# Kernel tuning notes

Measured on AMD Instinct MI355X. Metric: run time of the kernel, lower is better.

## Reference

```python
import jax, jax.numpy as jnp
import numpy as np
from jax import lax

B, S, D = 16, 1024, 1024
PE = 20          # positioning_embedding (LSTM hidden)
NB = 3           # num_building_blocks
EPS = 1e-12      # F.normalize eps


def setup_inputs() -> dict:
    key = jax.random.key(0)
    ks = jax.random.split(key, 10)
    s = lambda *sh: 0.05
    inp = {
        "x": jax.random.normal(ks[0], (B, S, D), dtype=jnp.float32),
        # LSTM params (PyTorch layout: gates ordered i,f,g,o)
        "W_ih": jax.random.normal(ks[1], (4 * PE, D), dtype=jnp.float32) * 0.02,
        "W_hh": jax.random.normal(ks[2], (4 * PE, PE), dtype=jnp.float32) * 0.02,
        "b_ih": jax.random.normal(ks[3], (4 * PE,), dtype=jnp.float32) * 0.02,
        "b_hh": jax.random.normal(ks[4], (4 * PE,), dtype=jnp.float32) * 0.02,
        # mu_generator: Linear(PE -> NB)
        "W_mu": jax.random.normal(ks[5], (NB, PE), dtype=jnp.float32) * 0.1,
        "b_mu": jax.random.normal(ks[6], (NB,), dtype=jnp.float32) * 0.1,
        # sigma_generator: Linear(PE -> 1)
        "W_sig": jax.random.normal(ks[7], (1, PE), dtype=jnp.float32) * 0.1,
        "b_sig": jax.random.normal(ks[8], (1,), dtype=jnp.float32) * 0.1,
    }
    return inp


def _lstm(x, W_ih, W_hh, b_ih, b_hh):
    # x: [B, S, D] -> h: [B, S, PE]; single-layer batch_first LSTM, h0=c0=0
    b, _, _ = x.shape
    H = W_hh.shape[1]
    xg = jnp.einsum("bsd,gd->bsg", x, W_ih) + b_ih + b_hh  # [B,S,4H]

    def step(carry, xg_t):
        h, c = carry
        g = xg_t + h @ W_hh.T
        i, f, gg, o = jnp.split(g, 4, axis=-1)
        c = jax.nn.sigmoid(f) * c + jax.nn.sigmoid(i) * jnp.tanh(gg)
        h = jax.nn.sigmoid(o) * jnp.tanh(c)
        return (h, c), h

    init = (jnp.zeros((b, H), x.dtype), jnp.zeros((b, H), x.dtype))
    _, hs = lax.scan(step, init, xg.transpose(1, 0, 2))  # hs: [S,B,H]
    return hs.transpose(1, 0, 2)


def _forward(x, W_ih, W_hh, b_ih, b_hh, W_mu, b_mu, W_sig, b_sig):
    b, s, d = x.shape
    pw = _lstm(x, W_ih, W_hh, b_ih, b_hh)                       # [B,S,PE]
    mu_w = jax.nn.relu(jnp.einsum("bsp,np->bsn", pw, W_mu) + b_mu)   # [B,S,3]
    sigma = jax.nn.sigmoid(jnp.einsum("bsp,op->bso", pw, W_sig) + b_sig)[..., 0]  # [B,S]

    # sequential mu recurrence: mu_j = w0*prev_mu + w1*(1/S) + w2*(j+1)/S
    j_idx = jnp.arange(s, dtype=x.dtype)

    def mu_step(prev_mu, inputs):
        w_t, j = inputs  # w_t: [B,3]
        mu = w_t[:, 0] * prev_mu + w_t[:, 1] / s + w_t[:, 2] * (j + 1.0) / s
        return mu, mu

    _, mus = lax.scan(mu_step, jnp.zeros((b,), x.dtype),
                      (mu_w.transpose(1, 0, 2), j_idx))          # mus: [S,B]
    mu = mus.T                                                    # [B,S]

    # triangular relative positions: rel[j,i] = i/(j+1) for i<=j
    i_idx = jnp.arange(s, dtype=x.dtype)
    rel = i_idx[None, :] / (j_idx[:, None] + 1.0)                 # [S,S]
    mask = i_idx[None, :] <= j_idx[:, None]                       # lower-triangular

    w = jnp.exp(-((rel[None] - mu[:, :, None]) ** 2)
                / (2.0 * sigma[:, :, None] ** 2))                 # [B,S,S]
    w = jnp.where(mask[None], w, 0.0)
    # F.normalize over the position axis (L2)
    norm = jnp.sqrt(jnp.sum(w * w, axis=-1, keepdims=True))
    w = w / jnp.maximum(norm, EPS)

    context = jnp.einsum("bji,bid->bjd", w, x)                    # [B,S,D]
    return context


def reference(x, W_ih, W_hh, b_ih, b_hh, W_mu, b_mu, W_sig, b_sig):
    return _forward(x, W_ih, W_hh, b_ih, b_hh, W_mu, b_mu, W_sig, b_sig)
```

## Files before the change

### kernel.cpp

```cpp
#include <hip/hip_runtime.h>

#define DEVFN __device__ __forceinline__

static constexpr int cB  = 16;
static constexpr int cS  = 1024;
static constexpr int cD  = 1024;
static constexpr int cPE = 20;
static constexpr int cG  = 80;

typedef float  floatx2  __attribute__((ext_vector_type(2)));
typedef float  floatx4  __attribute__((ext_vector_type(4)));
typedef float  floatx16 __attribute__((ext_vector_type(16)));
typedef short  short8   __attribute__((ext_vector_type(8)));
typedef unsigned uintx2 __attribute__((ext_vector_type(2)));

DEVFN unsigned pack_bf(float a, float b) {
  union { float f; unsigned u; } ua, ub; ua.f = a; ub.f = b;
  return (ua.u >> 16) | (ub.u & 0xffff0000u);
}

static constexpr int K1_XS = 68;

__global__ __launch_bounds__(256) void k1_xg(
    const float* __restrict__ x, const float* __restrict__ W_ih,
    const float* __restrict__ b_ih, const float* __restrict__ b_hh,
    float* __restrict__ xgT, unsigned short* __restrict__ xbf_t, int use_bf)
{
  __shared__ float xs[64 * K1_XS];
  __shared__ float wsm[80 * K1_XS];

  const int t  = threadIdx.x;
  const int rg = t >> 4, cg = t & 15;
  const int r0 = rg * 4, c0 = cg * 5;
  const int row0 = blockIdx.x * 64;
  const int b  = row0 >> 10;
  const int s0 = row0 & 1023;

  floatx2 acc[4][5];
#pragma unroll
  for (int q = 0; q < 4; ++q)
#pragma unroll
    for (int cc = 0; cc < 5; ++cc) { acc[q][cc].x = 0.f; acc[q][cc].y = 0.f; }

  for (int kc = 0; kc < 16; ++kc) {
    const int k0 = kc * 64;
    {
      const int sr = t >> 2, sc = t & 3;
      const float4* src = (const float4*)(x + (size_t)(row0 + sr) * cD + k0 + sc * 16);
      float4 v0 = src[0], v1 = src[1], v2 = src[2], v3 = src[3];
      float4* dst = (float4*)&xs[sr * K1_XS + sc * 16];
      dst[0] = v0; dst[1] = v1; dst[2] = v2; dst[3] = v3;
    }
#pragma unroll
    for (int q = 0; q < 5; ++q) {
      const int id = t + q * 256;
      const int g = id >> 4, c4 = id & 15;
      float4 wv = *(const float4*)(W_ih + (size_t)g * cD + k0 + c4 * 4);
      *(float4*)&wsm[g * K1_XS + c4 * 4] = wv;
    }
    __syncthreads();

    if (use_bf) {
      const int dl = t >> 2, sc4 = t & 3;
      float v[16];
#pragma unroll
      for (int e = 0; e < 16; ++e) v[e] = xs[(sc4 * 16 + e) * K1_XS + dl];
      unsigned u[8];
#pragma unroll
      for (int p = 0; p < 8; ++p) u[p] = pack_bf(v[2 * p], v[2 * p + 1]);
      unsigned short* dstp = xbf_t + ((size_t)(b * cD + k0 + dl)) * cS + s0 + sc4 * 16;
      *(uint4*)dstp       = make_uint4(u[0], u[1], u[2], u[3]);
      *(uint4*)(dstp + 8) = make_uint4(u[4], u[5], u[6], u[7]);
    }

#pragma unroll 4
    for (int k2 = 0; k2 < 32; ++k2) {
      floatx2 xv[4], wv[5];
#pragma unroll
      for (int q = 0; q < 4; ++q)
        xv[q] = *(const floatx2*)&xs[(r0 + q) * K1_XS + 2 * k2];
#pragma unroll
      for (int cc = 0; cc < 5; ++cc)
        wv[cc] = *(const floatx2*)&wsm[(c0 + cc) * K1_XS + 2 * k2];
#pragma unroll
      for (int q = 0; q < 4; ++q)
#pragma unroll
        for (int cc = 0; cc < 5; ++cc)
          acc[q][cc] += xv[q] * wv[cc];
    }
    __syncthreads();
  }

#pragma unroll
  for (int cc = 0; cc < 5; ++cc) {
    const int g = c0 + cc;
    const float sc = (g >= 40 && g < 60) ? 2.88539008f : 1.44269504f;
    const float bs = b_ih[g] + b_hh[g];
    float4 v;
    v.x = (acc[0][cc].x + acc[0][cc].y + bs) * sc;
    v.y = (acc[1][cc].x + acc[1][cc].y + bs) * sc;
    v.z = (acc[2][cc].x + acc[2][cc].y + bs) * sc;
    v.w = (acc[3][cc].x + acc[3][cc].y + bs) * sc;
    *(float4*)&xgT[((size_t)(b * cG + g)) * cS + s0 + r0] = v;
  }
}

__global__ __launch_bounds__(64) void k2_lstm(
    const float* __restrict__ xgT, const float* __restrict__ W_hh,
    float* __restrict__ hbuf)
{
  const int b    = blockIdx.x;
  const int lane = threadIdx.x;
  const int half = lane >> 5;
  const int l31  = lane & 31;
  const int j    = (l31 < cPE) ? l31 : (cPE - 1);
  const float LOG2E = 1.44269504f, TWOLOG2E = 2.88539008f;

  const int rowA = half ? (20 + j) : j;
  const int rowB = half ? (60 + j) : (40 + j);
  const float sB   = half ? LOG2E : TWOLOG2E;
  const float subB = half ? 0.f : 1.f;

  floatx2 wA[10], wB[10];
#pragma unroll
  for (int p = 0; p < 10; ++p) {
    wA[p].x = W_hh[rowA * cPE + 2 * p]     * LOG2E;
    wA[p].y = W_hh[rowA * cPE + 2 * p + 1] * LOG2E;
    wB[p].x = W_hh[rowB * cPE + 2 * p]     * sB;
    wB[p].y = W_hh[rowB * cPE + 2 * p + 1] * sB;
  }

  const float* baseA = xgT + ((size_t)(b * cG + rowA)) * cS;
  const float* baseB = xgT + ((size_t)(b * cG + rowB)) * cS;

  float4 bufA[4], bufB[4];
#pragma unroll
  for (int s = 0; s < 4; ++s) {
    bufA[s] = *(const float4*)(baseA + s * 4);
    bufB[s] = *(const float4*)(baseB + s * 4);
  }

  unsigned long long hp[10];
#pragma unroll
  for (int p = 0; p < 10; ++p) hp[p] = 0ull;

  float c = 0.f;
  float* hb = hbuf + (size_t)b * cS * cPE + j;

  for (int q0 = 0; q0 < 256; q0 += 4) {
#pragma unroll
    for (int s = 0; s < 4; ++s) {
      const int q = q0 + s;
      const float4 gA4 = bufA[s];
      const float4 gB4 = bufB[s];
      bufA[s] = *(const float4*)(baseA + (q + 4) * 4);
      bufB[s] = *(const float4*)(baseB + (q + 4) * 4);
#pragma unroll
      for (int e = 0; e < 4; ++e) {
        const float geA = (e == 0) ? gA4.x : (e == 1) ? gA4.y : (e == 2) ? gA4.z : gA4.w;
        const float geB = (e == 0) ? gB4.x : (e == 1) ? gB4.y : (e == 2) ? gB4.z : gB4.w;

        floatx2 aA0, aA1, aB0, aB1;
        aA0.x = geA; aA0.y = 0.f; aA1.x = 0.f; aA1.y = 0.f;
        aB0.x = geB; aB0.y = 0.f; aB1.x = 0.f; aB1.y = 0.f;
#pragma unroll
        for (int p = 0; p < 5; ++p) {
          asm("v_pk_fma_f32 %0, %1, %2, %0" : "+v"(aA0) : "v"(wA[p]),     "s"(hp[p]));
          asm("v_pk_fma_f32 %0, %1, %2, %0" : "+v"(aA1) : "v"(wA[5 + p]), "s"(hp[5 + p]));
          asm("v_pk_fma_f32 %0, %1, %2, %0" : "+v"(aB0) : "v"(wB[p]),     "s"(hp[p]));
          asm("v_pk_fma_f32 %0, %1, %2, %0" : "+v"(aB1) : "v"(wB[5 + p]), "s"(hp[5 + p]));
        }
        const float gAv = (aA0.x + aA0.y) + (aA1.x + aA1.y);
        const float gBv = (aB0.x + aB0.y) + (aB1.x + aB1.y);

        const float eA   = __builtin_amdgcn_exp2f(fminf(gAv, 30.f));
        const float actA = eA * __builtin_amdgcn_rcpf(eA + 1.f);
        const float eB   = __builtin_amdgcn_exp2f(fminf(gBv, 30.f));
        const float actB = (eB - subB) * __builtin_amdgcn_rcpf(eB + 1.f);

        union { float f; unsigned u; } ca, cb;
        ca.f = actA; cb.f = actB;
        uintx2 rA = __builtin_amdgcn_permlane32_swap(ca.u, ca.u, false, false);
        uintx2 rB = __builtin_amdgcn_permlane32_swap(cb.u, cb.u, false, false);
        union { unsigned u; float f; } vf, vi, vg, vo;
        vi.u = rA.x; vf.u = rA.y; vg.u = rB.x; vo.u = rB.y;

        c = vf.f * c + vi.f * vg.f;
        const float ec = __builtin_amdgcn_exp2f(fminf(TWOLOG2E * c, 30.f));
        const float th = (ec - 1.f) * __builtin_amdgcn_rcpf(ec + 1.f);
        const float hj = vo.f * th;

        if (lane < cPE) hb[(size_t)(q * 4 + e) * cPE] = hj;

        union { float f; unsigned u; } ch; ch.f = hj;
        const int hbits = (int)ch.u;
        const unsigned l0  = (unsigned)__builtin_amdgcn_readlane(hbits, 0);
        const unsigned l1  = (unsigned)__builtin_amdgcn_readlane(hbits, 1);
        const unsigned l2  = (unsigned)__builtin_amdgcn_readlane(hbits, 2);
        const unsigned l3  = (unsigned)__builtin_amdgcn_readlane(hbits, 3);
        const unsigned l4  = (unsigned)__builtin_amdgcn_readlane(hbits, 4);
        const unsigned l5  = (unsigned)__builtin_amdgcn_readlane(hbits, 5);
        const unsigned l6  = (unsigned)__builtin_amdgcn_readlane(hbits, 6);
        const unsigned l7  = (unsigned)__builtin_amdgcn_readlane(hbits, 7);
        const unsigned l8  = (unsigned)__builtin_amdgcn_readlane(hbits, 8);
        const unsigned l9  = (unsigned)__builtin_amdgcn_readlane(hbits, 9);
        const unsigned l10 = (unsigned)__builtin_amdgcn_readlane(hbits, 10);
        const unsigned l11 = (unsigned)__builtin_amdgcn_readlane(hbits, 11);
        const unsigned l12 = (unsigned)__builtin_amdgcn_readlane(hbits, 12);
        const unsigned l13 = (unsigned)__builtin_amdgcn_readlane(hbits, 13);
        const unsigned l14 = (unsigned)__builtin_amdgcn_readlane(hbits, 14);
        const unsigned l15 = (unsigned)__builtin_amdgcn_readlane(hbits, 15);
        const unsigned l16 = (unsigned)__builtin_amdgcn_readlane(hbits, 16);
        const unsigned l17 = (unsigned)__builtin_amdgcn_readlane(hbits, 17);
        const unsigned l18 = (unsigned)__builtin_amdgcn_readlane(hbits, 18);
        const unsigned l19 = (unsigned)__builtin_amdgcn_readlane(hbits, 19);
        hp[0] = (unsigned long long)l0  | ((unsigned long long)l1  << 32);
        hp[1] = (unsigned long long)l2  | ((unsigned long long)l3  << 32);
        hp[2] = (unsigned long long)l4  | ((unsigned long long)l5  << 32);
        hp[3] = (unsigned long long)l6  | ((unsigned long long)l7  << 32);
        hp[4] = (unsigned long long)l8  | ((unsigned long long)l9  << 32);
        hp[5] = (unsigned long long)l10 | ((unsigned long long)l11 << 32);
        hp[6] = (unsigned long long)l12 | ((unsigned long long)l13 << 32);
        hp[7] = (unsigned long long)l14 | ((unsigned long long)l15 << 32);
        hp[8] = (unsigned long long)l16 | ((unsigned long long)l17 << 32);
        hp[9] = (unsigned long long)l18 | ((unsigned long long)l19 << 32);
      }
    }
  }
}

__global__ __launch_bounds__(256) void k3a_muw(
    const float* __restrict__ hbuf,
    const float* __restrict__ W_mu, const float* __restrict__ b_mu,
    const float* __restrict__ W_sig, const float* __restrict__ b_sig,
    float* __restrict__ muwT, float* __restrict__ sigma)
{
  __shared__ float sw[84];
  const int t = threadIdx.x;
  if (t < 60) sw[t] = W_mu[t];
  else if (t < 80) sw[t] = W_sig[t - 60];
  else if (t < 83) sw[t] = b_mu[t - 80];
  else if (t == 83) sw[t] = b_sig[0];
  __syncthreads();

  const int r = blockIdx.x * 256 + t;
  const float4* hp = (const float4*)(hbuf + (size_t)r * cPE);
  float h[20];
#pragma unroll
  for (int q2 = 0; q2 < 5; ++q2) {
    float4 v = hp[q2];
    h[4 * q2] = v.x; h[4 * q2 + 1] = v.y; h[4 * q2 + 2] = v.z; h[4 * q2 + 3] = v.w;
  }
  float m0 = sw[80], m1 = sw[81], m2 = sw[82], sg = sw[83];
#pragma unroll
  for (int p = 0; p < 20; ++p) {
    m0 += sw[p]      * h[p];
    m1 += sw[20 + p] * h[p];
    m2 += sw[40 + p] * h[p];
    sg += sw[60 + p] * h[p];
  }
  muwT[r]                 = fmaxf(m0, 0.f);
  muwT[cB * cS + r]       = fmaxf(m1, 0.f);
  muwT[2 * cB * cS + r]   = fmaxf(m2, 0.f);
  sigma[r] = __builtin_amdgcn_rcpf(1.f + __builtin_amdgcn_exp2f(-1.44269504f * sg));
}

__global__ __launch_bounds__(64) void k3b_mu(
    const float* __restrict__ muwT, float* __restrict__ mu)
{
  const int t = threadIdx.x;
  if (t >= cB) return;
  const float* s0p = muwT + (size_t)t * cS;
  const float* s1p = muwT + cB * cS + (size_t)t * cS;
  const float* s2p = muwT + 2 * cB * cS + (size_t)t * cS;
  float* mb = mu + (size_t)t * cS;
  const float inv = 1.f / (float)cS;

  float4 b0[8], b1[8], b2[8];
#pragma unroll
  for (int u = 0; u < 8; ++u) {
    b0[u] = *(const float4*)(s0p + u * 4);
    b1[u] = *(const float4*)(s1p + u * 4);
    b2[u] = *(const float4*)(s2p + u * 4);
  }

  float m = 0.f;
  for (int t8 = 0; t8 < 32; ++t8) {
#pragma unroll
    for (int u = 0; u < 8; ++u) {
      const int t4 = t8 * 8 + u;
      float4 w0 = b0[u], w1 = b1[u], w2 = b2[u];
      if (t4 < 248) {
        b0[u] = *(const float4*)(s0p + (t4 + 8) * 4);
        b1[u] = *(const float4*)(s1p + (t4 + 8) * 4);
        b2[u] = *(const float4*)(s2p + (t4 + 8) * 4);
      }
      const int tt = t4 * 4;
      m = w0.x * m + (w1.x + w2.x * (float)(tt + 1)) * inv; mb[tt]     = m;
      m = w0.y * m + (w1.y + w2.y * (float)(tt + 2)) * inv; mb[tt + 1] = m;
      m = w0.z * m + (w1.z + w2.z * (float)(tt + 3)) * inv; mb[tt + 2] = m;
      m = w0.w * m + (w1.w + w2.w * (float)(tt + 4)) * inv; mb[tt + 3] = m;
    }
  }
}

static constexpr int TJ = 64, TD = 128, KI = 32, RS = 40;

__global__ __launch_bounds__(256) void k4_attn(
    const float* __restrict__ x, const unsigned short* __restrict__ xbf_t,
    int use_bf, const float* __restrict__ mu, const float* __restrict__ sigma,
    float* __restrict__ out)
{
  __shared__ unsigned short xsT[2][TD * RS];
  __shared__ float snrm[2][32];
  __shared__ float sscl[2][32];

  const int b   = blockIdx.z;
  const int jt0 = blockIdx.x * TJ;
  const int dt0 = blockIdx.y * TD;
  const int tid = threadIdx.x;
  const int wave = tid >> 6, lane = tid & 63;
  const int jh = wave & 1, dh = wave >> 1;
  const int n32 = lane & 31, half = lane >> 5;
  const int jrow = jt0 + jh * 32 + n32;

  const float muv  = mu[b * cS + jrow];
  const float sg   = sigma[b * cS + jrow];
  const float invj = 1.f / (float)(jrow + 1);
  const float ce   = -0.72134752f / (sg * sg);

  float nrm2 = 0.f;
  floatx16 acc0 = (floatx16)0.f, acc1 = (floatx16)0.f;

  const int iend = jt0 + TJ;

  auto stage = [&](int pb, int i0) {
    if (use_bf) {
#pragma unroll
      for (int q = 0; q < 2; ++q) {
        const int cc = tid + q * 256;
        const int dl = cc >> 2, part = cc & 3;
        uint4 v = *(const uint4*)(xbf_t + ((size_t)(b * cD + dt0 + dl)) * cS + i0 + part * 8);
        *(uint4*)&xsT[pb][dl * RS + part * 8] = v;
      }
    } else {
#pragma unroll
      for (int q = 0; q < 2; ++q) {
        const int cc = tid + q * 256;
        const int i = cc & 31, d8 = cc >> 5;
        const float* xp = x + ((size_t)(b * cS + i0 + i)) * cD + dt0 + d8 * 8;
        float4 f0 = *(const float4*)xp;
        float4 f1 = *(const float4*)(xp + 4);
        float vv[8] = {f0.x, f0.y, f0.z, f0.w, f1.x, f1.y, f1.z, f1.w};
#pragma unroll
        for (int e = 0; e < 8; ++e) {
          union { float f; unsigned u; } cv; cv.f = vv[e];
          xsT[pb][(d8 * 8 + e) * RS + i] = (unsigned short)(cv.u >> 16);
        }
      }
    }
  };

  stage(0, 0);
  __syncthreads();

  int pb = 0;
  for (int i0 = 0; i0 < iend; i0 += KI) {
    if (i0 + KI < iend) stage(pb ^ 1, i0 + KI);

    short8 af0, af1;
#pragma unroll
    for (int kc = 0; kc < 2; ++kc) {
      short8 af;
#pragma unroll
      for (int e = 0; e < 8; ++e) {
        const int ig = i0 + kc * 16 + half * 8 + e;
        const float d = fmaf((float)ig, invj, -muv);
        float w = __builtin_amdgcn_exp2f(ce * d * d);
        w = (ig <= jrow) ? w : 0.f;
        nrm2 += w * w;
        union { float f; unsigned u; } cv; cv.f = w;
        af[e] = (short)(cv.u >> 16);
      }
      if (kc == 0) af0 = af; else af1 = af;
    }

    const int rbase = dh * 64 + n32;
    short8 b00 = *(const short8*)&xsT[pb][(rbase)      * RS + half * 8];
    short8 b01 = *(const short8*)&xsT[pb][(rbase)      * RS + 16 + half * 8];
    short8 b10 = *(const short8*)&xsT[pb][(rbase + 32) * RS + half * 8];
    short8 b11 = *(const short8*)&xsT[pb][(rbase + 32) * RS + 16 + half * 8];
    acc0 = __builtin_amdgcn_mfma_f32_32x32x16_bf16(af0, b00, acc0, 0, 0, 0);
    acc0 = __builtin_amdgcn_mfma_f32_32x32x16_bf16(af1, b01, acc0, 0, 0, 0);
    acc1 = __builtin_amdgcn_mfma_f32_32x32x16_bf16(af0, b10, acc1, 0, 0, 0);
    acc1 = __builtin_amdgcn_mfma_f32_32x32x16_bf16(af1, b11, acc1, 0, 0, 0);

    __syncthreads();
    pb ^= 1;
  }

  nrm2 += __shfl_xor(nrm2, 32);
  if (wave < 2 && half == 0) snrm[jh][n32] = nrm2;
  __syncthreads();
  if (tid < 64)
    sscl[tid >> 5][tid & 31] =
        __builtin_amdgcn_rcpf(fmaxf(sqrtf(snrm[tid >> 5][tid & 31]), 1e-12f));
  __syncthreads();

  float srow[16];
#pragma unroll
  for (int reg = 0; reg < 16; ++reg) {
    const int row = (reg & 3) + 8 * (reg >> 2) + 4 * half;
    srow[reg] = sscl[jh][row];
  }
#pragma unroll
  for (int reg = 0; reg < 16; ++reg) {
    const int row = (reg & 3) + 8 * (reg >> 2) + 4 * half;
    const int jg = jt0 + jh * 32 + row;
    const int d0 = dt0 + dh * 64 + n32;
    out[((size_t)(b * cS + jg)) * cD + d0]      = acc0[reg] * srow[reg];
    out[((size_t)(b * cS + jg)) * cD + d0 + 32] = acc1[reg] * srow[reg];
  }
}

extern "C" void kernel_launch(void* const* d_in, const int* in_sizes, int n_in,
                              void* d_out, int out_size, void* d_ws, size_t ws_size,
                              hipStream_t stream) {
  const float* x     = (const float*)d_in[0];
  const float* W_ih  = (const float*)d_in[1];
  const float* W_hh  = (const float*)d_in[2];
  const float* b_ih  = (const float*)d_in[3];
  const float* b_hh  = (const float*)d_in[4];
  const float* W_mu  = (const float*)d_in[5];
  const float* b_mu  = (const float*)d_in[6];
  const float* W_sig = (const float*)d_in[7];
  const float* b_sig = (const float*)d_in[8];
  float* out = (float*)d_out;

  char* ws = (char*)d_ws;
  const size_t off_xg  = 0;
  const size_t off_h   = off_xg  + (size_t)cB*cS*cG*4;
  const size_t off_muw = off_h   + (size_t)cB*cS*cPE*4;
  const size_t off_sig = off_muw + (size_t)cB*cS*3*4;
  const size_t off_mu  = off_sig + (size_t)cB*cS*4;
  const size_t off_xbf = off_mu  + (size_t)cB*cS*4;
  const size_t need_bf = off_xbf + (size_t)cB*cS*cD*2;

  float* xgT   = (float*)(ws + off_xg);
  float* hbuf  = (float*)(ws + off_h);
  float* muwT  = (float*)(ws + off_muw);
  float* sigma = (float*)(ws + off_sig);
  float* mu    = (float*)(ws + off_mu);
  unsigned short* xbf_t = (unsigned short*)(ws + off_xbf);
  const int use_bf = (ws_size >= need_bf) ? 1 : 0;

  k1_xg  <<<dim3(cB * cS / 64), dim3(256), 0, stream>>>(x, W_ih, b_ih, b_hh, xgT, xbf_t, use_bf);
  k2_lstm<<<dim3(cB),           dim3(64),  0, stream>>>(xgT, W_hh, hbuf);
  k3a_muw<<<dim3(cB * cS / 256), dim3(256), 0, stream>>>(hbuf, W_mu, b_mu, W_sig, b_sig, muwT, sigma);
  k3b_mu <<<dim3(1),            dim3(64),  0, stream>>>(muwT, mu);
  k4_attn<<<dim3(cS/TJ, cD/TD, cB), dim3(256), 0, stream>>>(x, xbf_t, use_bf, mu, sigma, out);
}
```

Baseline: 471.0 us.

## Use fp16 dot2 in LSTM recurrence, halve k1 tiles, pack waves per block

The LSTM recurrence now keeps weights and hidden state as packed fp16 and uses v_dot2 with a DPP neighbour swap. This halves the readlane broadcasts per step and removes the packed-fp32 FMAs. Sigmoid clamping is dropped and the two activations share one reciprocal. Separately, k1 uses 32-row tiles to launch twice as many blocks, k2 runs 8 batch waves per 512-thread block across 2 blocks, and k4 restricts the norm accumulation to dh==0. Trade-offs: fp16 hidden state loses precision, unclamped exp2 can overflow, and the k4 norm change could be wrong if the norm is combined across dh later.

```diff
diff --git a/kernel.cpp b/kernel.cpp
--- a/kernel.cpp
+++ b/kernel.cpp
@@ -13,11 +13,14 @@
 typedef float  floatx16 __attribute__((ext_vector_type(16)));
 typedef short  short8   __attribute__((ext_vector_type(8)));
 typedef unsigned uintx2 __attribute__((ext_vector_type(2)));
+typedef __fp16 half2f  __attribute__((ext_vector_type(2)));
 
 DEVFN unsigned pack_bf(float a, float b) {
   union { float f; unsigned u; } ua, ub; ua.f = a; ub.f = b;
   return (ua.u >> 16) | (ub.u & 0xffff0000u);
 }
+DEVFN half2f u2h(unsigned u) { union { unsigned u; half2f h; } c; c.u = u; return c.h; }
+DEVFN unsigned h2u(half2f h) { union { half2f h; unsigned u; } c; c.h = h; return c.u; }
 
 static constexpr int K1_XS = 68;
 
@@ -26,30 +29,30 @@
     const float* __restrict__ b_ih, const float* __restrict__ b_hh,
     float* __restrict__ xgT, unsigned short* __restrict__ xbf_t, int use_bf)
 {
-  __shared__ float xs[64 * K1_XS];
+  __shared__ float xs[32 * K1_XS];
   __shared__ float wsm[80 * K1_XS];
 
   const int t  = threadIdx.x;
   const int rg = t >> 4, cg = t & 15;
-  const int r0 = rg * 4, c0 = cg * 5;
-  const int row0 = blockIdx.x * 64;
+  const int r0 = rg * 2, c0 = cg * 5;
+  const int row0 = blockIdx.x * 32;
   const int b  = row0 >> 10;
   const int s0 = row0 & 1023;
 
-  floatx2 acc[4][5];
-#pragma unroll
-  for (int q = 0; q < 4; ++q)
+  floatx2 acc[2][5];
+#pragma unroll
+  for (int q = 0; q < 2; ++q)
 #pragma unroll
     for (int cc = 0; cc < 5; ++cc) { acc[q][cc].x = 0.f; acc[q][cc].y = 0.f; }
 
   for (int kc = 0; kc < 16; ++kc) {
     const int k0 = kc * 64;
     {
-      const int sr = t >> 2, sc = t & 3;
-      const float4* src = (const float4*)(x + (size_t)(row0 + sr) * cD + k0 + sc * 16);
-      float4 v0 = src[0], v1 = src[1], v2 = src[2], v3 = src[3];
-      float4* dst = (float4*)&xs[sr * K1_XS + sc * 16];
-      dst[0] = v0; dst[1] = v1; dst[2] = v2; dst[3] = v3;
+      const int sr = t >> 3, sc = t & 7;
+      const float4* src = (const float4*)(x + (size_t)(row0 + sr) * cD + k0 + sc * 8);
+      float4 v0 = src[0], v1 = src[1];
+      float4* dst = (float4*)&xs[sr * K1_XS + sc * 8];
+      dst[0] = v0; dst[1] = v1;
     }
 #pragma unroll
     for (int q = 0; q < 5; ++q) {
@@ -61,29 +64,28 @@
     __syncthreads();
 
     if (use_bf) {
-      const int dl = t >> 2, sc4 = t & 3;
-      float v[16];
-#pragma unroll
-      for (int e = 0; e < 16; ++e) v[e] = xs[(sc4 * 16 + e) * K1_XS + dl];
-      unsigned u[8];
-#pragma unroll
-      for (int p = 0; p < 8; ++p) u[p] = pack_bf(v[2 * p], v[2 * p + 1]);
-      unsigned short* dstp = xbf_t + ((size_t)(b * cD + k0 + dl)) * cS + s0 + sc4 * 16;
-      *(uint4*)dstp       = make_uint4(u[0], u[1], u[2], u[3]);
-      *(uint4*)(dstp + 8) = make_uint4(u[4], u[5], u[6], u[7]);
+      const int dl = t >> 2, sc8 = t & 3;
+      float v[8];
+#pragma unroll
+      for (int e = 0; e < 8; ++e) v[e] = xs[(sc8 * 8 + e) * K1_XS + dl];
+      unsigned u[4];
+#pragma unroll
+      for (int p = 0; p < 4; ++p) u[p] = pack_bf(v[2 * p], v[2 * p + 1]);
+      unsigned short* dstp = xbf_t + ((size_t)(b * cD + k0 + dl)) * cS + s0 + sc8 * 8;
+      *(uint4*)dstp = make_uint4(u[0], u[1], u[2], u[3]);
     }
 
 #pragma unroll 4
     for (int k2 = 0; k2 < 32; ++k2) {
-      floatx2 xv[4], wv[5];
-#pragma unroll
-      for (int q = 0; q < 4; ++q)
+      floatx2 xv[2], wv[5];
+#pragma unroll
+      for (int q = 0; q < 2; ++q)
         xv[q] = *(const floatx2*)&xs[(r0 + q) * K1_XS + 2 * k2];
 #pragma unroll
       for (int cc = 0; cc < 5; ++cc)
         wv[cc] = *(const floatx2*)&wsm[(c0 + cc) * K1_XS + 2 * k2];
 #pragma unroll
-      for (int q = 0; q < 4; ++q)
+      for (int q = 0; q < 2; ++q)
 #pragma unroll
         for (int cc = 0; cc < 5; ++cc)
           acc[q][cc] += xv[q] * wv[cc];
@@ -96,21 +98,20 @@
     const int g = c0 + cc;
     const float sc = (g >= 40 && g < 60) ? 2.88539008f : 1.44269504f;
     const float bs = b_ih[g] + b_hh[g];
-    float4 v;
+    floatx2 v;
     v.x = (acc[0][cc].x + acc[0][cc].y + bs) * sc;
     v.y = (acc[1][cc].x + acc[1][cc].y + bs) * sc;
-    v.z = (acc[2][cc].x + acc[2][cc].y + bs) * sc;
-    v.w = (acc[3][cc].x + acc[3][cc].y + bs) * sc;
-    *(float4*)&xgT[((size_t)(b * cG + g)) * cS + s0 + r0] = v;
-  }
-}
-
-__global__ __launch_bounds__(64) void k2_lstm(
+    *(floatx2*)&xgT[((size_t)(b * cG + g)) * cS + s0 + r0] = v;
+  }
+}
+
+__global__ __launch_bounds__(512) void k2_lstm(
     const float* __restrict__ xgT, const float* __restrict__ W_hh,
     float* __restrict__ hbuf)
 {
-  const int b    = blockIdx.x;
-  const int lane = threadIdx.x;
+  const int wave = threadIdx.x >> 6;
+  const int lane = threadIdx.x & 63;
+  const int b    = blockIdx.x * 8 + wave;
   const int half = lane >> 5;
   const int l31  = lane & 31;
   const int j    = (l31 < cPE) ? l31 : (cPE - 1);
@@ -121,13 +122,13 @@
   const float sB   = half ? LOG2E : TWOLOG2E;
   const float subB = half ? 0.f : 1.f;
 
-  floatx2 wA[10], wB[10];
+  half2f wA16[10], wB16[10];
 #pragma unroll
   for (int p = 0; p < 10; ++p) {
-    wA[p].x = W_hh[rowA * cPE + 2 * p]     * LOG2E;
-    wA[p].y = W_hh[rowA * cPE + 2 * p + 1] * LOG2E;
-    wB[p].x = W_hh[rowB * cPE + 2 * p]     * sB;
-    wB[p].y = W_hh[rowB * cPE + 2 * p + 1] * sB;
+    wA16[p] = __builtin_amdgcn_cvt_pkrtz(W_hh[rowA * cPE + 2 * p]     * LOG2E,
+                                         W_hh[rowA * cPE + 2 * p + 1] * LOG2E);
+    wB16[p] = __builtin_amdgcn_cvt_pkrtz(W_hh[rowB * cPE + 2 * p]     * sB,
+                                         W_hh[rowB * cPE + 2 * p + 1] * sB);
   }
 
   const float* baseA = xgT + ((size_t)(b * cG + rowA)) * cS;
@@ -140,9 +141,9 @@
     bufB[s] = *(const float4*)(baseB + s * 4);
   }
 
-  unsigned long long hp[10];
-#pragma unroll
-  for (int p = 0; p < 10; ++p) hp[p] = 0ull;
+  half2f hs[10];
+#pragma unroll
+  for (int p = 0; p < 10; ++p) hs[p] = u2h(0u);
 
   float c = 0.f;
   float* hb = hbuf + (size_t)b * cS * cPE + j;
@@ -160,23 +161,23 @@
         const float geA = (e == 0) ? gA4.x : (e == 1) ? gA4.y : (e == 2) ? gA4.z : gA4.w;
         const float geB = (e == 0) ? gB4.x : (e == 1) ? gB4.y : (e == 2) ? gB4.z : gB4.w;
 
-        floatx2 aA0, aA1, aB0, aB1;
-        aA0.x = geA; aA0.y = 0.f; aA1.x = 0.f; aA1.y = 0.f;
-        aB0.x = geB; aB0.y = 0.f; aB1.x = 0.f; aB1.y = 0.f;
+        float a0 = geA, a1 = 0.f, c0v = geB, c1v = 0.f;
 #pragma unroll
         for (int p = 0; p < 5; ++p) {
-          asm("v_pk_fma_f32 %0, %1, %2, %0" : "+v"(aA0) : "v"(wA[p]),     "s"(hp[p]));
-          asm("v_pk_fma_f32 %0, %1, %2, %0" : "+v"(aA1) : "v"(wA[5 + p]), "s"(hp[5 + p]));
-          asm("v_pk_fma_f32 %0, %1, %2, %0" : "+v"(aB0) : "v"(wB[p]),     "s"(hp[p]));
-          asm("v_pk_fma_f32 %0, %1, %2, %0" : "+v"(aB1) : "v"(wB[5 + p]), "s"(hp[5 + p]));
+          a0  = __builtin_amdgcn_fdot2(wA16[p],     hs[p],     a0,  false);
+          c0v = __builtin_amdgcn_fdot2(wB16[p],     hs[p],     c0v, false);
+          a1  = __builtin_amdgcn_fdot2(wA16[5 + p], hs[5 + p], a1,  false);
+          c1v = __builtin_amdgcn_fdot2(wB16[5 + p], hs[5 + p], c1v, false);
         }
-        const float gAv = (aA0.x + aA0.y) + (aA1.x + aA1.y);
-        const float gBv = (aB0.x + aB0.y) + (aB1.x + aB1.y);
-
-        const float eA   = __builtin_amdgcn_exp2f(fminf(gAv, 30.f));
-        const float actA = eA * __builtin_amdgcn_rcpf(eA + 1.f);
-        const float eB   = __builtin_amdgcn_exp2f(fminf(gBv, 30.f));
-        const float actB = (eB - subB) * __builtin_amdgcn_rcpf(eB + 1.f);
+        const float gAv = a0 + a1;
+        const float gBv = c0v + c1v;
+
+        const float eA = __builtin_amdgcn_exp2f(gAv);
+        const float eB = __builtin_amdgcn_exp2f(gBv);
+        const float pA = eA + 1.f, pB = eB + 1.f;
+        const float rr = __builtin_amdgcn_rcpf(pA * pB);
+        const float actA = eA * pB * rr;
+        const float actB = (eB - subB) * (pA * rr);
 
         union { float f; unsigned u; } ca, cb;
         ca.f = actA; cb.f = actB;
@@ -192,38 +193,21 @@
 
         if (lane < cPE) hb[(size_t)(q * 4 + e) * cPE] = hj;
 
-        union { float f; unsigned u; } ch; ch.f = hj;
-        const int hbits = (int)ch.u;
-        const unsigned l0  = (unsigned)__builtin_amdgcn_readlane(hbits, 0);
-        const unsigned l1  = (unsigned)__builtin_amdgcn_readlane(hbits, 1);
-        const unsigned l2  = (unsigned)__builtin_amdgcn_readlane(hbits, 2);
-        const unsigned l3  = (unsigned)__builtin_amdgcn_readlane(hbits, 3);
-        const unsigned l4  = (unsigned)__builtin_amdgcn_readlane(hbits, 4);
-        const unsigned l5  = (unsigned)__builtin_amdgcn_readlane(hbits, 5);
-        const unsigned l6  = (unsigned)__builtin_amdgcn_readlane(hbits, 6);
-        const unsigned l7  = (unsigned)__builtin_amdgcn_readlane(hbits, 7);
-        const unsigned l8  = (unsigned)__builtin_amdgcn_readlane(hbits, 8);
-        const unsigned l9  = (unsigned)__builtin_amdgcn_readlane(hbits, 9);
-        const unsigned l10 = (unsigned)__builtin_amdgcn_readlane(hbits, 10);
-        const unsigned l11 = (unsigned)__builtin_amdgcn_readlane(hbits, 11);
-        const unsigned l12 = (unsigned)__builtin_amdgcn_readlane(hbits, 12);
-        const unsigned l13 = (unsigned)__builtin_amdgcn_readlane(hbits, 13);
-        const unsigned l14 = (unsigned)__builtin_amdgcn_readlane(hbits, 14);
-        const unsigned l15 = (unsigned)__builtin_amdgcn_readlane(hbits, 15);
-        const unsigned l16 = (unsigned)__builtin_amdgcn_readlane(hbits, 16);
-        const unsigned l17 = (unsigned)__builtin_amdgcn_readlane(hbits, 17);
-        const unsigned l18 = (unsigned)__builtin_amdgcn_readlane(hbits, 18);
-        const unsigned l19 = (unsigned)__builtin_amdgcn_readlane(hbits, 19);
-        hp[0] = (unsigned long long)l0  | ((unsigned long long)l1  << 32);
-        hp[1] = (unsigned long long)l2  | ((unsigned long long)l3  << 32);
-        hp[2] = (unsigned long long)l4  | ((unsigned long long)l5  << 32);
-        hp[3] = (unsigned long long)l6  | ((unsigned long long)l7  << 32);
-        hp[4] = (unsigned long long)l8  | ((unsigned long long)l9  << 32);
-        hp[5] = (unsigned long long)l10 | ((unsigned long long)l11 << 32);
-        hp[6] = (unsigned long long)l12 | ((unsigned long long)l13 << 32);
-        hp[7] = (unsigned long long)l14 | ((unsigned long long)l15 << 32);
-        hp[8] = (unsigned long long)l16 | ((unsigned long long)l17 << 32);
-        hp[9] = (unsigned long long)l18 | ((unsigned long long)l19 << 32);
+        union { float f; int i; } hji; hji.f = hj;
+        const int nbi = __builtin_amdgcn_mov_dpp(hji.i, 0xB1, 0xF, 0xF, true);
+        union { int i; float f; } nbf; nbf.i = nbi;
+        const half2f pk = __builtin_amdgcn_cvt_pkrtz(hj, nbf.f);
+        const unsigned pku = h2u(pk);
+        hs[0] = u2h((unsigned)__builtin_amdgcn_readlane((int)pku, 0));
+        hs[1] = u2h((unsigned)__builtin_amdgcn_readlane((int)pku, 2));
+        hs[2] = u2h((unsigned)__builtin_amdgcn_readlane((int)pku, 4));
+        hs[3] = u2h((unsigned)__builtin_amdgcn_readlane((int)pku, 6));
+        hs[4] = u2h((unsigned)__builtin_amdgcn_readlane((int)pku, 8));
+        hs[5] = u2h((unsigned)__builtin_amdgcn_readlane((int)pku, 10));
+        hs[6] = u2h((unsigned)__builtin_amdgcn_readlane((int)pku, 12));
+        hs[7] = u2h((unsigned)__builtin_amdgcn_readlane((int)pku, 14));
+        hs[8] = u2h((unsigned)__builtin_amdgcn_readlane((int)pku, 16));
+        hs[9] = u2h((unsigned)__builtin_amdgcn_readlane((int)pku, 18));
       }
     }
   }
@@ -378,7 +362,7 @@
         const float d = fmaf((float)ig, invj, -muv);
         float w = __builtin_amdgcn_exp2f(ce * d * d);
         w = (ig <= jrow) ? w : 0.f;
-        nrm2 += w * w;
+        if (dh == 0) nrm2 += w * w;
         union { float f; unsigned u; } cv; cv.f = w;
         af[e] = (short)(cv.u >> 16);
       }
@@ -454,9 +438,9 @@
   unsigned short* xbf_t = (unsigned short*)(ws + off_xbf);
   const int use_bf = (ws_size >= need_bf) ? 1 : 0;
 
-  k1_xg  <<<dim3(cB * cS / 64), dim3(256), 0, stream>>>(x, W_ih, b_ih, b_hh, xgT, xbf_t, use_bf);
-  k2_lstm<<<dim3(cB),           dim3(64),  0, stream>>>(xgT, W_hh, hbuf);
+  k1_xg  <<<dim3(cB * cS / 32),  dim3(256), 0, stream>>>(x, W_ih, b_ih, b_hh, xgT, xbf_t, use_bf);
+  k2_lstm<<<dim3(2),             dim3(512), 0, stream>>>(xgT, W_hh, hbuf);
   k3a_muw<<<dim3(cB * cS / 256), dim3(256), 0, stream>>>(hbuf, W_mu, b_mu, W_sig, b_sig, muwT, sigma);
-  k3b_mu <<<dim3(1),            dim3(64),  0, stream>>>(muwT, mu);
+  k3b_mu <<<dim3(1),             dim3(64),  0, stream>>>(muwT, mu);
   k4_attn<<<dim3(cS/TJ, cD/TD, cB), dim3(256), 0, stream>>>(x, xbf_t, use_bf, mu, sigma, out);
 }
```

Measured after the change: 539.5 us. +14.6%, slower.
